# Optimization experiments

Hardware: AMD Instinct MI355X
Metric: run time of the kernel (lower is better)

The kernel has to match this reference:

```python
import jax, jax.numpy as jnp
import numpy as np

WS = 8
HEADS = 8


def _conv3(x, w, groups=1):
    return jax.lax.conv_general_dilated(
        x, w, (1, 1), 'SAME',
        dimension_numbers=('NCHW', 'OIHW', 'NCHW'),
        feature_group_count=groups)


def _bn(x, g, b, eps=1e-5):
    # training-mode batchnorm (batch statistics), per-channel over (B,H,W)
    m = x.mean(axis=(0, 2, 3), keepdims=True)
    v = x.var(axis=(0, 2, 3), keepdims=True)
    return (x - m) * jax.lax.rsqrt(v + eps) * g[None, :, None, None] + b[None, :, None, None]


def _relu6(x):
    return jnp.clip(x, 0.0, 6.0)


def _forward(x, w_iem, g_iem, b_iem, w_nem, g_nem, b_nem,
             w_iem_dw, w_nem_dw, w_q, w_k, w_v, w_proj, temperature):
    b, C, hp, wp = x.shape
    heads = temperature.shape[1]
    d = C // heads
    ws = WS
    nh, nw = hp // ws, wp // ws  # H,W chosen divisible by ws -> no padding

    iem_out = _relu6(_bn(_conv3(x, w_iem), g_iem, b_iem))
    illumination_map = _conv3(iem_out, w_iem_dw, groups=C)
    nem_out = _relu6(_bn(_conv3(x, w_nem), g_nem, b_nem))
    noise_map = _conv3(nem_out, w_nem_dw, groups=C)

    illum_scalar = illumination_map.mean(axis=1, keepdims=True)  # [b,1,H,W]
    noise_scalar = noise_map.mean(axis=1, keepdims=True)

    # 1x1 convs as channel matmuls
    q = jnp.einsum('oc,bchw->bohw', w_q, illumination_map)
    k = jnp.einsum('oc,bchw->bohw', w_k, noise_map)
    v = jnp.einsum('oc,bchw->bohw', w_v, x)

    def to_windows(t):  # [b,C,H,W] -> [b,heads,nh,nw,ws*ws,d]
        t = t.reshape(b, heads, d, hp, wp).transpose(0, 1, 3, 4, 2)
        t = t.reshape(b, heads, nh, ws, nw, ws, d).transpose(0, 1, 2, 4, 3, 5, 6)
        return t.reshape(b, heads, nh, nw, ws * ws, d)

    def scalar_to_windows(t):  # [b,1,H,W] -> [b,1,nh,nw,ws*ws,1]
        t = t.reshape(b, 1, nh, ws, nw, ws).transpose(0, 1, 2, 4, 3, 5)
        return t.reshape(b, 1, nh, nw, ws * ws, 1)

    qw, kw, vw = to_windows(q), to_windows(k), to_windows(v)
    illum_w = scalar_to_windows(illum_scalar)
    noise_w = scalar_to_windows(noise_scalar)

    qw = qw / jnp.maximum(jnp.linalg.norm(qw, axis=-1, keepdims=True), 1e-12)
    kw = kw / jnp.maximum(jnp.linalg.norm(kw, axis=-1, keepdims=True), 1e-12)
    qw = qw * (1.0 + illum_w)
    kw = kw * jnp.clip(1.0 - noise_w, 0.0, 1.0)

    scale = d ** (-0.5)
    attn = jnp.einsum('bhnmqd,bhnmkd->bhnmqk', qw, kw) * scale
    attn = attn * temperature  # temperature: [1,heads,1,1,1,1]
    attn = jax.nn.softmax(attn, axis=-1)
    outw = jnp.einsum('bhnmqk,bhnmkd->bhnmqd', attn, vw)

    outw = outw.reshape(b, heads, nh, nw, ws, ws, d).transpose(0, 1, 6, 2, 4, 3, 5)
    out = outw.reshape(b, C, hp, wp)
    return jnp.einsum('oc,bchw->bohw', w_proj, out)


def setup_inputs() -> dict:
    key = jax.random.key(0)
    ks = jax.random.split(key, 10)
    C = 256
    B, H, W = 2, 256, 256

    def w(k, shape):
        return jax.random.normal(k, shape, jnp.float32) * 0.05

    return {
        'x': jax.random.normal(ks[0], (B, C, H, W), jnp.float32),
        'w_iem': w(ks[1], (C, C, 3, 3)),
        'g_iem': jnp.ones((C,), jnp.float32),
        'b_iem': jnp.zeros((C,), jnp.float32),
        'w_nem': w(ks[2], (C, C, 3, 3)),
        'g_nem': jnp.ones((C,), jnp.float32),
        'b_nem': jnp.zeros((C,), jnp.float32),
        'w_iem_dw': w(ks[3], (C, 1, 3, 3)),
        'w_nem_dw': w(ks[4], (C, 1, 3, 3)),
        'w_q': w(ks[5], (C, C)),
        'w_k': w(ks[6], (C, C)),
        'w_v': w(ks[7], (C, C)),
        'w_proj': w(ks[8], (C, C)),
        'temperature': jnp.ones((1, HEADS, 1, 1, 1, 1), jnp.float32),
    }


def reference(x, w_iem, g_iem, b_iem, w_nem, g_nem, b_nem,
              w_iem_dw, w_nem_dw, w_q, w_k, w_v, w_proj, temperature):
    return _forward(x, w_iem, g_iem, b_iem, w_nem, g_nem, b_nem,
                    w_iem_dw, w_nem_dw, w_q, w_k, w_v, w_proj, temperature)
```

## Files before the change

kernel.cpp:

```cpp
#include <hip/hip_runtime.h>
#include <math.h>

constexpr int Bn  = 2;
constexpr int C   = 256;
constexpr int H   = 256;
constexpr int W   = 256;
constexpr int HW  = H * W;
constexpr size_t CHW = (size_t)C * HW;

typedef __bf16 bf16x8 __attribute__((ext_vector_type(8)));
typedef float  f32x4  __attribute__((ext_vector_type(4)));

__device__ __forceinline__ unsigned short f2bf(float f) {
    unsigned int u = __float_as_uint(f);
    u += 0x7fffu + ((u >> 16) & 1u);
    return (unsigned short)(u >> 16);
}
__device__ __forceinline__ float bf2f(unsigned short h) {
    return __uint_as_float(((unsigned int)h) << 16);
}
__device__ __forceinline__ float bflo(unsigned int u) { return __uint_as_float(u << 16); }
__device__ __forceinline__ float bfhi(unsigned int u) { return __uint_as_float(u & 0xffff0000u); }

__device__ __forceinline__ bf16x8 u2b(uint4 u) {
    union { uint4 a; bf16x8 b; } c; c.a = u; return c.b;
}

__device__ __forceinline__ void gld_lds16(const void* g, void* lds) {
    __builtin_amdgcn_global_load_lds(
        (const __attribute__((address_space(1))) unsigned int*)g,
        (__attribute__((address_space(3))) unsigned int*)lds, 16, 0, 0);
}

__device__ __forceinline__ int swz2048(int bid) {
    return ((bid & 7) << 8) | (bid >> 3);
}

__global__ __launch_bounds__(256) void packx_k(
    const float* __restrict__ x, unsigned short* __restrict__ xT)
{
    __shared__ float tl[64][65];
    const int id = blockIdx.x;
    const int ct = id & 3;
    const size_t px0 = (size_t)(id >> 2) * 64;
    const int b  = (int)(px0 >> 16);
    const int hw = (int)(px0 & 65535);
    const int c0 = ct * 64;
    const int t  = threadIdx.x;

    {
        const int cl = t >> 2, pseg = t & 3;
        const float* src = x + ((size_t)(b * C + c0 + cl)) * HW + hw + pseg * 16;
#pragma unroll
        for (int i = 0; i < 4; i++) {
            float4 v = *(const float4*)(src + i * 4);
            tl[cl][pseg * 16 + i * 4 + 0] = v.x;
            tl[cl][pseg * 16 + i * 4 + 1] = v.y;
            tl[cl][pseg * 16 + i * 4 + 2] = v.z;
            tl[cl][pseg * 16 + i * 4 + 3] = v.w;
        }
    }
    __syncthreads();
    {
        const int pl = t >> 2, csec = t & 3;
        __attribute__((aligned(16))) unsigned short rv[16];
#pragma unroll
        for (int j = 0; j < 16; j++) rv[j] = f2bf(tl[csec * 16 + j][pl]);
        unsigned short* dst = xT + (px0 + pl) * C + c0 + csec * 16;
        *(uint4*)dst       = *(const uint4*)&rv[0];
        *(uint4*)(dst + 8) = *(const uint4*)&rv[8];
    }
}

__global__ __launch_bounds__(256) void pack_k(
    const float* __restrict__ w, unsigned short* __restrict__ out, int taps)
{
    const int e = blockIdx.x * 256 + threadIdx.x;
    const int kslot = e & 31;
    const int ocl   = (e >> 5) & 127;
    const int icc   = (e >> 12) & 7;
    const int oct   = (e >> 15) & 1;
    const int off   = e >> 16;
    const int oc = oct * 128 + ocl;
    const int q  = kslot >> 3, j = kslot & 7;
    const int ic = icc * 32 + ((q ^ ((ocl >> 2) & 3)) << 3) + j;
    out[e] = f2bf(w[((size_t)oc * C + ic) * taps + off]);
}

__global__ __launch_bounds__(256) void pack4_k(
    const float* __restrict__ wq, const float* __restrict__ wk,
    const float* __restrict__ wv, const float* __restrict__ wp,
    unsigned short* __restrict__ oq, unsigned short* __restrict__ ok,
    unsigned short* __restrict__ ov, unsigned short* __restrict__ op)
{
    const int bid  = blockIdx.x;
    const int wsel = bid >> 8;
    const int e    = (bid & 255) * 256 + threadIdx.x;
    const float* w = (wsel == 0) ? wq : (wsel == 1) ? wk : (wsel == 2) ? wv : wp;
    unsigned short* out = (wsel == 0) ? oq : (wsel == 1) ? ok : (wsel == 2) ? ov : op;
    const int kslot = e & 31;
    const int ocl   = (e >> 5) & 127;
    const int icc   = (e >> 12) & 7;
    const int oct   = (e >> 15) & 1;
    const int oc = oct * 128 + ocl;
    const int q  = kslot >> 3, j = kslot & 7;
    const int ic = icc * 32 + ((q ^ ((ocl >> 2) & 3)) << 3) + j;
    out[e] = f2bf(w[(size_t)oc * C + ic]);
}

__global__ __launch_bounds__(256, 2) void conv2_k(
    const unsigned short* __restrict__ xT,
    const unsigned short* __restrict__ Wp0, const unsigned short* __restrict__ Wp1,
    unsigned short* __restrict__ out0, unsigned short* __restrict__ out1,
    const unsigned short* __restrict__ zbuf, float* __restrict__ stats_part)
{
    __shared__ unsigned short As[3][2][128 * 32];
    __shared__ unsigned short Bs[136 * 32];
    __shared__ float sstat[2][128][2];

    const int id  = swz2048(blockIdx.x);
    const int oct = id & 1;
    const int ch  = (id >> 1) & 1;
    const int r   = (id >> 2) & 255;
    const int b   = id >> 10;
    const int px0 = ch * 128;

    const int t  = threadIdx.x;
    const int wv = t >> 6;
    const int l  = t & 63;
    const int wm = (wv >> 1) * 64;
    const int wn = (wv & 1) * 64;
    const int g  = l >> 4;

    ((float*)sstat)[t]       = 0.f;
    ((float*)sstat)[t + 256] = 0.f;

    const int qp = (l >> 4) ^ ((l >> 2) & 3);
    int a_off[4];
#pragma unroll
    for (int i = 0; i < 4; i++)
        a_off[i] = (wm + i * 16 + (l & 15)) * 64 + qp * 16;

    const int dy_lo = (r == 0) ? 1 : 0;
    const int dy_hi = (r == 255) ? 1 : 2;

    f32x4 acc[2][4][4];
#pragma unroll
    for (int s = 0; s < 2; s++)
#pragma unroll
        for (int i = 0; i < 4; i++)
#pragma unroll
            for (int j = 0; j < 4; j++) acc[s][i][j] = (f32x4){0.f, 0.f, 0.f, 0.f};

#pragma unroll 1
    for (int dy = dy_lo; dy <= dy_hi; ++dy) {
        const int rr = r + dy - 1;
        const size_t rowpix = (size_t)(b * HW) + (size_t)rr * W;
#pragma unroll 1
        for (int icc = 0; icc < 8; ++icc) {
            __syncthreads();
#pragma unroll
            for (int dxt = 0; dxt < 3; dxt++) {
                const int off = dy * 3 + dxt;
                const size_t wofs = ((size_t)(((off * 2 + oct) * 8 + icc)) * 4096) * 2
                                    + wv * 2048 + l * 16;
                char* A0 = (char*)As[dxt][0] + wv * 2048;
                char* A1 = (char*)As[dxt][1] + wv * 2048;
                gld_lds16((const char*)Wp0 + wofs, A0);
                gld_lds16((const char*)Wp0 + wofs + 1024, A0 + 1024);
                gld_lds16((const char*)Wp1 + wofs, A1);
                gld_lds16((const char*)Wp1 + wofs + 1024, A1 + 1024);
            }
            const int ic0 = icc * 32;
#pragma unroll
            for (int i = 0; i < 2; i++) {
                const int j   = wv * 16 + (l >> 2) + i * 64;
                const int gpx = px0 + j - 1;
                const int kg  = (l & 3) ^ ((j >> 2) & 3);
                const void* gsrc = ((unsigned)gpx > 255u)
                    ? (const void*)zbuf
                    : (const void*)(xT + ((rowpix + gpx) * C + ic0 + kg * 8));
                gld_lds16(gsrc, (char*)Bs + wv * 1024 + i * 4096);
            }
            if (t < 8) {
                const int j   = 128 + (l >> 2);
                const int gpx = px0 + j - 1;
                const int kg  = (l & 3) ^ ((j >> 2) & 3);
                const void* gsrc = ((unsigned)gpx > 255u)
                    ? (const void*)zbuf
                    : (const void*)(xT + ((rowpix + gpx) * C + ic0 + kg * 8));
                gld_lds16(gsrc, (char*)Bs + 8192);
            }
            asm volatile("s_waitcnt vmcnt(0)" ::: "memory");
            __syncthreads();
#pragma unroll
            for (int dxt = 0; dxt < 3; dxt++) {
                bf16x8 bfr[4];
#pragma unroll
                for (int i = 0; i < 4; i++) {
                    const int j  = wn + i * 16 + (l & 15) + dxt;
                    const int bq = g ^ ((j >> 2) & 3);
                    bfr[i] = *(const bf16x8*)((const char*)Bs + j * 64 + bq * 16);
                }
                bf16x8 af0[4], af1[4];
#pragma unroll
                for (int i = 0; i < 4; i++) {
                    af0[i] = *(const bf16x8*)((const char*)As[dxt][0] + a_off[i]);
                    af1[i] = *(const bf16x8*)((const char*)As[dxt][1] + a_off[i]);
                }
#pragma unroll
                for (int mi = 0; mi < 4; mi++)
#pragma unroll
                    for (int nj = 0; nj < 4; nj++) {
                        acc[0][mi][nj] = __builtin_amdgcn_mfma_f32_16x16x32_bf16(
                            af0[mi], bfr[nj], acc[0][mi][nj], 0, 0, 0);
                        acc[1][mi][nj] = __builtin_amdgcn_mfma_f32_16x16x32_bf16(
                            af1[mi], bfr[nj], acc[1][mi][nj], 0, 0, 0);
                    }
            }
        }
    }

    const int colpx = px0 + wn + (l & 15);
    const int rowoc = oct * 128 + wm + (l >> 4) * 4;
#pragma unroll
    for (int s = 0; s < 2; s++) {
        unsigned short* ob = s ? out1 : out0;
#pragma unroll
        for (int mi = 0; mi < 4; mi++) {
#pragma unroll
            for (int rg = 0; rg < 4; rg++) {
                const int oc = rowoc + mi * 16 + rg;
                float ps = 0.f, pq = 0.f;
#pragma unroll
                for (int nj = 0; nj < 4; nj++) {
                    const float v = acc[s][mi][nj][rg];
                    ps += v;
                    pq = fmaf(v, v, pq);
                    const int px = colpx + nj * 16;
                    const size_t idx = ((size_t)(b * C + oc)) * HW + (size_t)r * W + px;
                    ob[idx] = f2bf(v);
                }
                ps += __shfl_xor(ps, 1);  pq += __shfl_xor(pq, 1);
                ps += __shfl_xor(ps, 2);  pq += __shfl_xor(pq, 2);
                ps += __shfl_xor(ps, 4);  pq += __shfl_xor(pq, 4);
                ps += __shfl_xor(ps, 8);  pq += __shfl_xor(pq, 8);
                if ((l & 15) == 0) {
                    const int loc = wm + (l >> 4) * 4 + mi * 16 + rg;
                    atomicAdd(&sstat[s][loc][0], ps);
                    atomicAdd(&sstat[s][loc][1], pq);
                }
            }
        }
    }
    __syncthreads();
    stats_part[(size_t)id * 512 + t * 2 + 0] = ((float(*)[2])sstat)[t][0];
    stats_part[(size_t)id * 512 + t * 2 + 1] = ((float(*)[2])sstat)[t][1];
}

__global__ __launch_bounds__(256) void bn_reduce_k(
    const float* __restrict__ stats_part,
    const float* __restrict__ g0, const float* __restrict__ b0,
    const float* __restrict__ g1, const float* __restrict__ b1,
    float* __restrict__ scl0, float* __restrict__ shf0,
    float* __restrict__ scl1, float* __restrict__ shf1)
{
    const int s   = blockIdx.x >> 8;
    const int gc  = blockIdx.x & 255;
    const int oct = gc >> 7;
    const int loc = gc & 127;
    const int t   = threadIdx.x;
    const int ent = (s * 128 + loc) * 2;

    float ps = 0.f, pq = 0.f;
#pragma unroll
    for (int m = 0; m < 4; m++) {
        const int id = oct + 2 * (t + 256 * m);
        ps += stats_part[(size_t)id * 512 + ent];
        pq += stats_part[(size_t)id * 512 + ent + 1];
    }
    __shared__ float rs[256], rq[256];
    rs[t] = ps; rq[t] = pq;
    __syncthreads();
    for (int o = 128; o > 0; o >>= 1) {
        if (t < o) { rs[t] += rs[t + o]; rq[t] += rq[t + o]; }
        __syncthreads();
    }
    if (t == 0) {
        const float n    = (float)Bn * HW;
        const float mean = rs[0] / n;
        const float var  = rq[0] / n - mean * mean;
        const float g    = s ? g1[gc] : g0[gc];
        const float be   = s ? b1[gc] : b0[gc];
        const float sc   = g * rsqrtf(var + 1e-5f);
        if (s) { scl1[gc] = sc; shf1[gc] = be - mean * sc; }
        else   { scl0[gc] = sc; shf0[gc] = be - mean * sc; }
    }
}

__global__ __launch_bounds__(256, 2) void gemm2_k(
    const unsigned short* __restrict__ qin, const unsigned short* __restrict__ kin,
    const unsigned short* __restrict__ Wpq, const unsigned short* __restrict__ Wpk,
    unsigned short* __restrict__ outq, unsigned short* __restrict__ outk)
{
    __shared__ unsigned short As[2][2][128 * 32];
    __shared__ unsigned short Bs[2][2][128 * 32];

    const int id  = swz2048(blockIdx.x);
    const int oct = id & 1;
    const int ch  = (id >> 1) & 1;
    const int r   = (id >> 2) & 255;
    const int b   = id >> 10;
    const int px0 = ch * 128;

    const int t  = threadIdx.x;
    const int wv = t >> 6;
    const int l  = t & 63;
    const int wm = (wv >> 1) * 64;
    const int wn = (wv & 1) * 64;

    const int qp = (l >> 4) ^ ((l >> 2) & 3);
    int a_off[4], b_off[4];
#pragma unroll
    for (int i = 0; i < 4; i++) {
        a_off[i] = (wm + i * 16 + (l & 15)) * 64 + qp * 16;
        b_off[i] = (wn + i * 16 + (l & 15)) * 64 + qp * 16;
    }
    const int spx_base = wv * 32 + (l >> 2);
    const int skk0 = (((l & 3) ^ (l >> 4)) << 3);

    const size_t rowpix = (size_t)(b * HW) + (size_t)r * W;

    f32x4 acc[2][4][4];
#pragma unroll
    for (int s = 0; s < 2; s++)
#pragma unroll
        for (int i = 0; i < 4; i++)
#pragma unroll
            for (int j = 0; j < 4; j++) acc[s][i][j] = (f32x4){0.f, 0.f, 0.f, 0.f};

#pragma unroll 1
    for (int ip = 0; ip < 4; ++ip) {
        __syncthreads();
#pragma unroll
        for (int kc = 0; kc < 2; kc++) {
            const int icc = ip * 2 + kc;
            const size_t wofs = ((size_t)(oct * 8 + icc) * 4096) * 2 + wv * 2048 + l * 16;
            char* Aq = (char*)As[0][kc] + wv * 2048;
            char* Ak = (char*)As[1][kc] + wv * 2048;
            gld_lds16((const char*)Wpq + wofs, Aq);
            gld_lds16((const char*)Wpq + wofs + 1024, Aq + 1024);
            gld_lds16((const char*)Wpk + wofs, Ak);
            gld_lds16((const char*)Wpk + wofs + 1024, Ak + 1024);
            const int ic0 = icc * 32;
            char* Bq = (char*)Bs[0][kc] + wv * 2048;
            char* Bk = (char*)Bs[1][kc] + wv * 2048;
#pragma unroll
            for (int i = 0; i < 2; i++) {
                const int cx = px0 + spx_base + i * 16;
                gld_lds16((const void*)(qin + ((rowpix + cx) * C + ic0 + skk0)), Bq + i * 1024);
                gld_lds16((const void*)(kin + ((rowpix + cx) * C + ic0 + skk0)), Bk + i * 1024);
            }
        }
        asm volatile("s_waitcnt vmcnt(0)" ::: "memory");
        __syncthreads();
#pragma unroll
        for (int kc = 0; kc < 2; kc++) {
#pragma unroll
            for (int s = 0; s < 2; s++) {
                bf16x8 af[4], bfr[4];
#pragma unroll
                for (int i = 0; i < 4; i++) {
                    af[i]  = *(const bf16x8*)((const char*)As[s][kc] + a_off[i]);
                    bfr[i] = *(const bf16x8*)((const char*)Bs[s][kc] + b_off[i]);
                }
#pragma unroll
                for (int mi = 0; mi < 4; mi++)
#pragma unroll
                    for (int nj = 0; nj < 4; nj++)
                        acc[s][mi][nj] = __builtin_amdgcn_mfma_f32_16x16x32_bf16(
                            af[mi], bfr[nj], acc[s][mi][nj], 0, 0, 0);
            }
        }
    }

    const int colpx = px0 + wn + (l & 15);
    const int rowoc = oct * 128 + wm + (l >> 4) * 4;
    const size_t pxg = (size_t)(b * HW) + (size_t)r * W;
#pragma unroll
    for (int s = 0; s < 2; s++) {
        unsigned short* ob = s ? outk : outq;
#pragma unroll
        for (int mi = 0; mi < 4; mi++) {
#pragma unroll
            for (int nj = 0; nj < 4; nj++) {
                __attribute__((aligned(8))) unsigned short rv[4];
#pragma unroll
                for (int rg = 0; rg < 4; rg++) rv[rg] = f2bf(acc[s][mi][nj][rg]);
                const int oc = rowoc + mi * 16;
                const int px = colpx + nj * 16;
                *(uint2*)(ob + (pxg + px) * C + oc) = *(const uint2*)rv;
            }
        }
    }
}

template<bool F32OUT, bool NHWC_OUT>
__global__ __launch_bounds__(256, 4) void gemm_k(
    const unsigned short* __restrict__ xT, const unsigned short* __restrict__ Wp,
    unsigned short* __restrict__ outb, float* __restrict__ outf)
{
    __shared__ unsigned short As[2][128 * 32];
    __shared__ unsigned short Bs[2][128 * 32];

    const int id  = swz2048(blockIdx.x);
    const int oct = id & 1;
    const int ch  = (id >> 1) & 1;
    const int r   = (id >> 2) & 255;
    const int b   = id >> 10;
    const int px0 = ch * 128;

    const int t  = threadIdx.x;
    const int wv = t >> 6;
    const int l  = t & 63;
    const int wm = (wv >> 1) * 64;
    const int wn = (wv & 1) * 64;

    const int qp = (l >> 4) ^ ((l >> 2) & 3);
    int a_off[4], b_off[4];
#pragma unroll
    for (int i = 0; i < 4; i++) {
        a_off[i] = (wm + i * 16 + (l & 15)) * 64 + qp * 16;
        b_off[i] = (wn + i * 16 + (l & 15)) * 64 + qp * 16;
    }
    const int spx_base = wv * 32 + (l >> 2);
    const int skk0 = (((l & 3) ^ (l >> 4)) << 3);

    const size_t rowpix = (size_t)(b * HW) + (size_t)r * W;

    f32x4 acc[4][4];
#pragma unroll
    for (int i = 0; i < 4; i++)
#pragma unroll
        for (int j = 0; j < 4; j++) acc[i][j] = (f32x4){0.f, 0.f, 0.f, 0.f};

#pragma unroll 1
    for (int ip = 0; ip < 4; ++ip) {
        __syncthreads();
#pragma unroll
        for (int kc = 0; kc < 2; kc++) {
            const int icc = ip * 2 + kc;
            const char* Ag = (const char*)Wp +
                ((size_t)(oct * 8 + icc) * 4096) * 2 + wv * 2048 + l * 16;
            char* AsB = (char*)As[kc] + wv * 2048;
            gld_lds16(Ag, AsB);
            gld_lds16(Ag + 1024, AsB + 1024);
            const int ic0 = icc * 32;
            char* BsB = (char*)Bs[kc] + wv * 2048;
#pragma unroll
            for (int i = 0; i < 2; i++) {
                const int cx = px0 + spx_base + i * 16;
                gld_lds16((const void*)(xT + ((rowpix + cx) * C + ic0 + skk0)), BsB + i * 1024);
            }
        }
        asm volatile("s_waitcnt vmcnt(0)" ::: "memory");
        __syncthreads();
#pragma unroll
        for (int kc = 0; kc < 2; kc++) {
            bf16x8 af[4], bfr[4];
#pragma unroll
            for (int i = 0; i < 4; i++) {
                af[i]  = *(const bf16x8*)((const char*)As[kc] + a_off[i]);
                bfr[i] = *(const bf16x8*)((const char*)Bs[kc] + b_off[i]);
            }
#pragma unroll
            for (int mi = 0; mi < 4; mi++)
#pragma unroll
                for (int nj = 0; nj < 4; nj++)
                    acc[mi][nj] = __builtin_amdgcn_mfma_f32_16x16x32_bf16(
                        af[mi], bfr[nj], acc[mi][nj], 0, 0, 0);
        }
    }

    const int colpx = px0 + wn + (l & 15);
    const int rowoc = oct * 128 + wm + (l >> 4) * 4;
    if (NHWC_OUT) {
        const size_t pxg = (size_t)(b * HW) + (size_t)r * W;
#pragma unroll
        for (int mi = 0; mi < 4; mi++) {
#pragma unroll
            for (int nj = 0; nj < 4; nj++) {
                __attribute__((aligned(8))) unsigned short rv[4];
#pragma unroll
                for (int rg = 0; rg < 4; rg++) rv[rg] = f2bf(acc[mi][nj][rg]);
                const int oc = rowoc + mi * 16;
                const int px = colpx + nj * 16;
                *(uint2*)(outb + (pxg + px) * C + oc) = *(const uint2*)rv;
            }
        }
    } else {
#pragma unroll
        for (int mi = 0; mi < 4; mi++) {
#pragma unroll
            for (int nj = 0; nj < 4; nj++) {
#pragma unroll
                for (int rg = 0; rg < 4; rg++) {
                    const int oc = rowoc + mi * 16 + rg;
                    const int px = colpx + nj * 16;
                    const size_t idx = ((size_t)(b * C + oc)) * HW + (size_t)r * W + px;
                    if (F32OUT) outf[idx] = acc[mi][nj][rg];
                    else        outb[idx] = f2bf(acc[mi][nj][rg]);
                }
            }
        }
    }
}

__global__ __launch_bounds__(256) void dwconv_k(
    const unsigned short* __restrict__ a0, const unsigned short* __restrict__ a1,
    const float* __restrict__ scl0, const float* __restrict__ shf0,
    const float* __restrict__ scl1, const float* __restrict__ shf1,
    const float* __restrict__ wd0, const float* __restrict__ wd1,
    unsigned short* __restrict__ out0, unsigned short* __restrict__ out1,
    float* __restrict__ sm0, float* __restrict__ sm1)
{
    __shared__ float tile[32][3][67];
    __shared__ float wds[32 * 9];
    __shared__ float sscl[32], sshf[32];

    const int id  = blockIdx.x;
    const int c0  = (id & 7) * 32;
    const int w0  = ((id >> 3) & 3) * 64;
    const int r   = (id >> 5) & 255;
    const int b   = (id >> 13) & 1;
    const int set = id >> 14;
    const int t   = threadIdx.x;

    const unsigned short* a   = set ? a1 : a0;
    const float* scale        = set ? scl1 : scl0;
    const float* shift        = set ? shf1 : shf0;
    const float* wd           = set ? wd1 : wd0;
    unsigned short* out       = set ? out1 : out0;
    float* smean              = set ? sm1 : sm0;

    for (int i = t; i < 288; i += 256) wds[i] = wd[c0 * 9 + i];
    if (t < 32) { sscl[t] = scale[c0 + t]; sshf[t] = shift[c0 + t]; }
    __syncthreads();

    for (int i = t; i < 1536; i += 256) {
        const int c   = i / 48;
        const int rem = i - c * 48;
        const int row = rem >> 4, seg = rem & 15;
        const int rr  = r + row - 1;
        float f0 = 0.f, f1 = 0.f, f2 = 0.f, f3 = 0.f;
        if ((unsigned)rr < 256u) {
            const uint2 v = *(const uint2*)(a + ((size_t)(b * C + c0 + c)) * HW
                                              + (size_t)rr * W + w0 + seg * 4);
            const float sc = sscl[c], sh = sshf[c];
            f0 = fminf(fmaxf(fmaf(bflo(v.x), sc, sh), 0.f), 6.f);
            f1 = fminf(fmaxf(fmaf(bfhi(v.x), sc, sh), 0.f), 6.f);
            f2 = fminf(fmaxf(fmaf(bflo(v.y), sc, sh), 0.f), 6.f);
            f3 = fminf(fmaxf(fmaf(bfhi(v.y), sc, sh), 0.f), 6.f);
        }
        float* dst = &tile[c][row][1 + seg * 4];
        dst[0] = f0; dst[1] = f1; dst[2] = f2; dst[3] = f3;
    }
    for (int i = t; i < 192; i += 256) {
        const int c   = i / 6;
        const int rem = i - c * 6;
        const int row = rem >> 1, side = rem & 1;
        const int rr  = r + row - 1;
        const int col = side ? (w0 + 64) : (w0 - 1);
        float v = 0.f;
        if ((unsigned)rr < 256u && (unsigned)col < 256u) {
            float u = bf2f(a[((size_t)(b * C + c0 + c)) * HW + (size_t)rr * W + col]);
            v = fminf(fmaxf(fmaf(u, sscl[c], sshf[c]), 0.f), 6.f);
        }
        tile[c][row][side ? 65 : 0] = v;
    }
    __syncthreads();

    const int px = t >> 2, csub = t & 3;
    __attribute__((aligned(16))) unsigned short res[8];
    float psum = 0.f;
#pragma unroll
    for (int k = 0; k < 8; k++) {
        const int c = csub * 8 + k;
        const float* wp = &wds[c * 9];
        float accv = 0.f;
#pragma unroll
        for (int dy = 0; dy < 3; dy++)
#pragma unroll
            for (int dx = 0; dx < 3; dx++)
                accv = fmaf(tile[c][dy][px + dx], wp[dy * 3 + dx], accv);
        res[k] = f2bf(accv);
        psum += accv;
    }
    unsigned short* o = out + ((size_t)(b * HW) + (size_t)r * W + w0 + px) * C + c0 + csub * 8;
    *(uint4*)o = *(const uint4*)&res[0];

    psum += __shfl_xor(psum, 1);
    psum += __shfl_xor(psum, 2);
    if (csub == 0)
        atomicAdd(&smean[(size_t)(b * HW) + (size_t)r * W + w0 + px], psum * (1.f / C));
}

__global__ __launch_bounds__(64) void attn_k(
    const unsigned short* __restrict__ q, const unsigned short* __restrict__ k,
    const unsigned short* __restrict__ v, const float* __restrict__ si,
    const float* __restrict__ sn, const float* __restrict__ temp,
    unsigned short* __restrict__ out)
{
    __shared__ unsigned short Pl[64][72];
    __shared__ unsigned short Vt[32][72];

    const int id   = blockIdx.x;
    const int wx   = id & 31;
    const int wy   = (id >> 5) & 31;
    const int head = (id >> 10) & 7;
    const int b    = id >> 13;
    const int l    = threadIdx.x;
    const int pl15 = l & 15;
    const int g    = l >> 4;
    const int ch0  = head * 32;
    const int base = wy * 8 * W + wx * 8;
    const size_t bb = (size_t)b * HW;

    uint4 qv[4], kv[4];
    float qss[4], kss[4];
#pragma unroll
    for (int i = 0; i < 4; i++) {
        const int p = i * 16 + pl15;
        const size_t a = (bb + base + (p >> 3) * W + (p & 7)) * C + ch0 + g * 8;
        qv[i] = *(const uint4*)(q + a);
        kv[i] = *(const uint4*)(k + a);
        float s0 = 0.f, s1 = 0.f;
        {
            uint4 u = qv[i];
            float f;
            f = bflo(u.x); s0 = fmaf(f, f, s0);  f = bfhi(u.x); s0 = fmaf(f, f, s0);
            f = bflo(u.y); s0 = fmaf(f, f, s0);  f = bfhi(u.y); s0 = fmaf(f, f, s0);
            f = bflo(u.z); s0 = fmaf(f, f, s0);  f = bfhi(u.z); s0 = fmaf(f, f, s0);
            f = bflo(u.w); s0 = fmaf(f, f, s0);  f = bfhi(u.w); s0 = fmaf(f, f, s0);
        }
        {
            uint4 u = kv[i];
            float f;
            f = bflo(u.x); s1 = fmaf(f, f, s1);  f = bfhi(u.x); s1 = fmaf(f, f, s1);
            f = bflo(u.y); s1 = fmaf(f, f, s1);  f = bfhi(u.y); s1 = fmaf(f, f, s1);
            f = bflo(u.z); s1 = fmaf(f, f, s1);  f = bfhi(u.z); s1 = fmaf(f, f, s1);
            f = bflo(u.w); s1 = fmaf(f, f, s1);  f = bfhi(u.w); s1 = fmaf(f, f, s1);
        }
        s0 += __shfl_xor(s0, 16); s0 += __shfl_xor(s0, 32);
        s1 += __shfl_xor(s1, 16); s1 += __shfl_xor(s1, 32);
        qss[i] = s0; kss[i] = s1;
    }

    {
        const size_t a = (bb + base + (l >> 3) * W + (l & 7)) * C + ch0;
        const uint4* vp = (const uint4*)(v + a);
#pragma unroll
        for (int i = 0; i < 4; i++) {
            uint4 vv = vp[i];
            Vt[i * 8 + 0][l] = (unsigned short)(vv.x);
            Vt[i * 8 + 1][l] = (unsigned short)(vv.x >> 16);
            Vt[i * 8 + 2][l] = (unsigned short)(vv.y);
            Vt[i * 8 + 3][l] = (unsigned short)(vv.y >> 16);
            Vt[i * 8 + 4][l] = (unsigned short)(vv.z);
            Vt[i * 8 + 5][l] = (unsigned short)(vv.z >> 16);
            Vt[i * 8 + 6][l] = (unsigned short)(vv.w);
            Vt[i * 8 + 7][l] = (unsigned short)(vv.w >> 16);
        }
    }

    const float tsc = temp[head] * 0.17677669529663689f;
    float qmul[4], kscl[4];
#pragma unroll
    for (int i = 0; i < 4; i++) {
        const int p = i * 16 + pl15;
        const size_t pg = bb + base + (p >> 3) * W + (p & 7);
        const float il = si[pg];
        const float nz = sn[pg];
        qmul[i] = (1.f + il) * tsc / fmaxf(sqrtf(qss[i]), 1e-12f);
        kscl[i] = fminf(fmaxf(1.f - nz, 0.f), 1.f) / fmaxf(sqrtf(kss[i]), 1e-12f);
    }

    f32x4 acc[4][4];
    __builtin_amdgcn_s_setprio(1);
#pragma unroll
    for (int qi = 0; qi < 4; qi++)
#pragma unroll
        for (int kj = 0; kj < 4; kj++)
            acc[qi][kj] = __builtin_amdgcn_mfma_f32_16x16x32_bf16(
                u2b(qv[qi]), u2b(kv[kj]), (f32x4){0.f, 0.f, 0.f, 0.f}, 0, 0, 0);
    __builtin_amdgcn_s_setprio(0);

    float inv[4][4];
#pragma unroll
    for (int qi = 0; qi < 4; qi++) {
#pragma unroll
        for (int rg = 0; rg < 4; rg++) {
            const float qm = __shfl(qmul[qi], (g << 2) + rg);
            float s[4];
#pragma unroll
            for (int kj = 0; kj < 4; kj++) s[kj] = acc[qi][kj][rg] * kscl[kj] * qm;
            float mx = fmaxf(fmaxf(s[0], s[1]), fmaxf(s[2], s[3]));
            mx = fmaxf(mx, __shfl_xor(mx, 1));
            mx = fmaxf(mx, __shfl_xor(mx, 2));
            mx = fmaxf(mx, __shfl_xor(mx, 4));
            mx = fmaxf(mx, __shfl_xor(mx, 8));
            float sum = 0.f;
#pragma unroll
            for (int kj = 0; kj < 4; kj++) {
                const float e = __expf(s[kj] - mx);
                acc[qi][kj][rg] = e;
                sum += e;
            }
            sum += __shfl_xor(sum, 1);
            sum += __shfl_xor(sum, 2);
            sum += __shfl_xor(sum, 4);
            sum += __shfl_xor(sum, 8);
            inv[qi][rg] = 1.f / sum;
            const int qrow = qi * 16 + (g << 2) + rg;
#pragma unroll
            for (int kj = 0; kj < 4; kj++)
                Pl[qrow][pl15 + 16 * kj] = f2bf(acc[qi][kj][rg]);
        }
    }

    f32x4 oacc[4][2];
#pragma unroll
    for (int qi = 0; qi < 4; qi++)
#pragma unroll
        for (int dj = 0; dj < 2; dj++) oacc[qi][dj] = (f32x4){0.f, 0.f, 0.f, 0.f};

#pragma unroll
    for (int kc = 0; kc < 2; kc++) {
        const bf16x8 vb0 = *(const bf16x8*)&Vt[pl15][kc * 32 + g * 8];
        const bf16x8 vb1 = *(const bf16x8*)&Vt[pl15 + 16][kc * 32 + g * 8];
        __builtin_amdgcn_s_setprio(1);
#pragma unroll
        for (int qi = 0; qi < 4; qi++) {
            const bf16x8 pa = *(const bf16x8*)&Pl[qi * 16 + pl15][kc * 32 + g * 8];
            oacc[qi][0] = __builtin_amdgcn_mfma_f32_16x16x32_bf16(pa, vb0, oacc[qi][0], 0, 0, 0);
            oacc[qi][1] = __builtin_amdgcn_mfma_f32_16x16x32_bf16(pa, vb1, oacc[qi][1], 0, 0, 0);
        }
        __builtin_amdgcn_s_setprio(0);
    }

#pragma unroll
    for (int qi = 0; qi < 4; qi++) {
#pragma unroll
        for (int rg = 0; rg < 4; rg++) {
            const int qrow = qi * 16 + (g << 2) + rg;
            const size_t oaddr = (bb + base + (qrow >> 3) * W + (qrow & 7)) * C + ch0;
            const float sc = inv[qi][rg];
            out[oaddr + pl15]      = f2bf(oacc[qi][0][rg] * sc);
            out[oaddr + 16 + pl15] = f2bf(oacc[qi][1][rg] * sc);
        }
    }
}

extern "C" void kernel_launch(void* const* d_in, const int* in_sizes, int n_in,
                              void* d_out, int out_size, void* d_ws, size_t ws_size,
                              hipStream_t stream)
{
    const float* x        = (const float*)d_in[0];
    const float* w_iem    = (const float*)d_in[1];
    const float* g_iem    = (const float*)d_in[2];
    const float* b_iem    = (const float*)d_in[3];
    const float* w_nem    = (const float*)d_in[4];
    const float* g_nem    = (const float*)d_in[5];
    const float* b_nem    = (const float*)d_in[6];
    const float* w_iem_dw = (const float*)d_in[7];
    const float* w_nem_dw = (const float*)d_in[8];
    const float* w_q      = (const float*)d_in[9];
    const float* w_k      = (const float*)d_in[10];
    const float* w_v      = (const float*)d_in[11];
    const float* w_proj   = (const float*)d_in[12];
    const float* temp     = (const float*)d_in[13];

    char* p = (char*)d_ws;
    unsigned short* zbuf = (unsigned short*)p;      p += 256;
    float* scl0 = (float*)p;                        p += 256 * 4;
    float* shf0 = (float*)p;                        p += 256 * 4;
    float* scl1 = (float*)p;                        p += 256 * 4;
    float* shf1 = (float*)p;                        p += 256 * 4;
    float* stats_part = (float*)p;                  p += (size_t)2048 * 512 * 4;
    float* sI  = (float*)p;                         p += (size_t)Bn * HW * 4;
    float* sN  = (float*)p;                         p += (size_t)Bn * HW * 4;
    unsigned short* Wp_iem = (unsigned short*)p;    p += 589824 * 2;
    unsigned short* Wp_nem = (unsigned short*)p;    p += 589824 * 2;
    unsigned short* Wpq = (unsigned short*)p;       p += 65536 * 2;
    unsigned short* Wpk = (unsigned short*)p;       p += 65536 * 2;
    unsigned short* Wpv = (unsigned short*)p;       p += 65536 * 2;
    unsigned short* Wpp = (unsigned short*)p;       p += 65536 * 2;
    unsigned short* xT   = (unsigned short*)p;      p += Bn * CHW * 2;
    unsigned short* bufA = (unsigned short*)p;      p += Bn * CHW * 2;
    unsigned short* Ibf  = (unsigned short*)p;      p += Bn * CHW * 2;
    unsigned short* Nbf  = (unsigned short*)p;      p += Bn * CHW * 2;
    unsigned short* Obf  = (unsigned short*)p;      p += Bn * CHW * 2;

    hipMemsetAsync(zbuf, 0, 256, stream);
    hipMemsetAsync(sI, 0, (size_t)Bn * HW * 4 * 2, stream);

    packx_k<<<8192, 256, 0, stream>>>(x, xT);
    pack_k<<<2304, 256, 0, stream>>>(w_iem, Wp_iem, 9);
    pack_k<<<2304, 256, 0, stream>>>(w_nem, Wp_nem, 9);
    pack4_k<<<1024, 256, 0, stream>>>(w_q, w_k, w_v, w_proj, Wpq, Wpk, Wpv, Wpp);

    conv2_k<<<2048, 256, 0, stream>>>(xT, Wp_iem, Wp_nem, bufA, Obf, zbuf, stats_part);
    bn_reduce_k<<<512, 256, 0, stream>>>(stats_part, g_iem, b_iem, g_nem, b_nem,
                                         scl0, shf0, scl1, shf1);

    dwconv_k<<<32768, 256, 0, stream>>>(bufA, Obf, scl0, shf0, scl1, shf1,
                                        w_iem_dw, w_nem_dw, Ibf, Nbf, sI, sN);

    gemm2_k<<<2048, 256, 0, stream>>>(Ibf, Nbf, Wpq, Wpk, bufA, Obf);
    gemm_k<false, true><<<2048, 256, 0, stream>>>(xT, Wpv, Nbf, nullptr);

    attn_k<<<16384, 64, 0, stream>>>(bufA, Obf, Nbf, sI, sN, temp, Ibf);

    gemm_k<true, false><<<2048, 256, 0, stream>>>(Ibf, Wpp, nullptr, (float*)d_out);
}
```

Baseline: 992.7 us.

## Store conv outputs channels-last and read them channels-last in depthwise stage

The conv GEMM epilogue now writes its bf16 output in NHWC layout, packing four consecutive channels into one 8-byte store instead of scattered 2-byte NCHW stores. The depthwise-conv tile loader reads that NHWC data with 16-byte loads of eight channels per pixel, which also merges the separate halo loop into the main loop. The point is better coalescing of the intermediate activation traffic. In exchange, the epilogue stores are strided by C across pixels, and the shared-tile writes are transposed, which may cause bank conflicts.

```diff
diff --git a/kernel.cpp b/kernel.cpp
--- a/kernel.cpp
+++ b/kernel.cpp
@@ -223,23 +223,29 @@
 
     const int colpx = px0 + wn + (l & 15);
     const int rowoc = oct * 128 + wm + (l >> 4) * 4;
+    const size_t pxg = (size_t)(b * HW) + (size_t)r * W;
 #pragma unroll
     for (int s = 0; s < 2; s++) {
         unsigned short* ob = s ? out1 : out0;
 #pragma unroll
         for (int mi = 0; mi < 4; mi++) {
 #pragma unroll
+            for (int nj = 0; nj < 4; nj++) {
+                __attribute__((aligned(8))) unsigned short rv[4];
+#pragma unroll
+                for (int rg = 0; rg < 4; rg++) rv[rg] = f2bf(acc[s][mi][nj][rg]);
+                const int oc = rowoc + mi * 16;
+                const int px = colpx + nj * 16;
+                *(uint2*)(ob + (pxg + px) * C + oc) = *(const uint2*)rv;
+            }
+#pragma unroll
             for (int rg = 0; rg < 4; rg++) {
-                const int oc = rowoc + mi * 16 + rg;
                 float ps = 0.f, pq = 0.f;
 #pragma unroll
                 for (int nj = 0; nj < 4; nj++) {
                     const float v = acc[s][mi][nj][rg];
                     ps += v;
                     pq = fmaf(v, v, pq);
-                    const int px = colpx + nj * 16;
-                    const size_t idx = ((size_t)(b * C + oc)) * HW + (size_t)r * W + px;
-                    ob[idx] = f2bf(v);
                 }
                 ps += __shfl_xor(ps, 1);  pq += __shfl_xor(pq, 1);
                 ps += __shfl_xor(ps, 2);  pq += __shfl_xor(pq, 2);
@@ -547,36 +553,30 @@
     if (t < 32) { sscl[t] = scale[c0 + t]; sshf[t] = shift[c0 + t]; }
     __syncthreads();
 
-    for (int i = t; i < 1536; i += 256) {
-        const int c   = i / 48;
-        const int rem = i - c * 48;
-        const int row = rem >> 4, seg = rem & 15;
+    for (int i = t; i < 792; i += 256) {
+        const int row = i / 264;
+        const int rem = i - row * 264;
+        const int pxc = rem >> 2;
+        const int ck  = rem & 3;
         const int rr  = r + row - 1;
-        float f0 = 0.f, f1 = 0.f, f2 = 0.f, f3 = 0.f;
-        if ((unsigned)rr < 256u) {
-            const uint2 v = *(const uint2*)(a + ((size_t)(b * C + c0 + c)) * HW
-                                              + (size_t)rr * W + w0 + seg * 4);
-            const float sc = sscl[c], sh = sshf[c];
-            f0 = fminf(fmaxf(fmaf(bflo(v.x), sc, sh), 0.f), 6.f);
-            f1 = fminf(fmaxf(fmaf(bfhi(v.x), sc, sh), 0.f), 6.f);
-            f2 = fminf(fmaxf(fmaf(bflo(v.y), sc, sh), 0.f), 6.f);
-            f3 = fminf(fmaxf(fmaf(bfhi(v.y), sc, sh), 0.f), 6.f);
-        }
-        float* dst = &tile[c][row][1 + seg * 4];
-        dst[0] = f0; dst[1] = f1; dst[2] = f2; dst[3] = f3;
-    }
-    for (int i = t; i < 192; i += 256) {
-        const int c   = i / 6;
-        const int rem = i - c * 6;
-        const int row = rem >> 1, side = rem & 1;
-        const int rr  = r + row - 1;
-        const int col = side ? (w0 + 64) : (w0 - 1);
-        float v = 0.f;
-        if ((unsigned)rr < 256u && (unsigned)col < 256u) {
-            float u = bf2f(a[((size_t)(b * C + c0 + c)) * HW + (size_t)rr * W + col]);
-            v = fminf(fmaxf(fmaf(u, sscl[c], sshf[c]), 0.f), 6.f);
-        }
-        tile[c][row][side ? 65 : 0] = v;
+        const int gpx = w0 - 1 + pxc;
+        const int cb  = ck * 8;
+        float f[8];
+#pragma unroll
+        for (int j = 0; j < 8; j++) f[j] = 0.f;
+        if ((unsigned)rr < 256u && (unsigned)gpx < 256u) {
+            const uint4 v = *(const uint4*)(a +
+                ((size_t)(b * HW) + (size_t)rr * W + gpx) * C + c0 + cb);
+            f[0] = bflo(v.x); f[1] = bfhi(v.x);
+            f[2] = bflo(v.y); f[3] = bfhi(v.y);
+            f[4] = bflo(v.z); f[5] = bfhi(v.z);
+            f[6] = bflo(v.w); f[7] = bfhi(v.w);
+#pragma unroll
+            for (int j = 0; j < 8; j++)
+                f[j] = fminf(fmaxf(fmaf(f[j], sscl[cb + j], sshf[cb + j]), 0.f), 6.f);
+        }
+#pragma unroll
+        for (int j = 0; j < 8; j++) tile[cb + j][row][pxc] = f[j];
     }
     __syncthreads();
 
```

Result: faster. 945.1 us (-4.8%).
